# Kernel tuning notes

Hardware: AMD Instinct MI355X
Metric: run time of the kernel (lower is better)

The kernel has to match this reference:

```python
import jax, jax.numpy as jnp
import numpy as np
import math

B, S, E = 8, 1024, 1024
H, D = 8, 1024  # n_heads, d_q=d_k=d_v (must equal S and E per broadcasting in the original)


def setup_inputs() -> dict:
    key = jax.random.key(0)
    ks = jax.random.split(key, 9)
    sc_in = 1.0 / math.sqrt(E)
    inputs = jax.random.normal(ks[0], (B, S, E), dtype=jnp.float32)
    Wq = jax.random.uniform(ks[1], (E, H * D), jnp.float32, -sc_in, sc_in)
    bq = jax.random.uniform(ks[2], (H * D,), jnp.float32, -sc_in, sc_in)
    Wk = jax.random.uniform(ks[3], (E, H * D), jnp.float32, -sc_in, sc_in)
    bk = jax.random.uniform(ks[4], (H * D,), jnp.float32, -sc_in, sc_in)
    Wv = jax.random.uniform(ks[5], (E, H * D), jnp.float32, -sc_in, sc_in)
    bv = jax.random.uniform(ks[6], (H * D,), jnp.float32, -sc_in, sc_in)
    WL = jax.random.uniform(ks[7], (E, H * D), jnp.float32, -sc_in, sc_in)
    bL = jax.random.uniform(ks[8], (H * D,), jnp.float32, -sc_in, sc_in)
    return {"inputs": inputs, "Wq": Wq, "bq": bq, "Wk": Wk, "bk": bk,
            "Wv": Wv, "bv": bv, "WL": WL, "bL": bL}


def reference(inputs, Wq, bq, Wk, bk, Wv, bv, WL, bL):
    b = inputs.shape[0]
    # projections -> [B, H, S, D]
    def proj(W, bias):
        return (inputs @ W + bias).reshape(b, S, H, D).transpose(0, 2, 1, 3)
    q = proj(Wq, bq)
    k = proj(Wk, bk)
    v = proj(Wv, bv)
    # elementwise "kv" score: [B,H,S,D] * [B,H,D,S] (D==S so shapes align) -> [B,H,S,S]
    kv = k * jnp.swapaxes(v, -1, -2) * jnp.float32(1.0 / math.sqrt(D))
    attn = jax.nn.softmax(kv, axis=2)          # softmax over non-standard axis 2
    pooled = jnp.sum(attn * q, axis=2)         # [B, H, S]  (S == E)
    return pooled @ WL + bL                    # [B, H, H*D]
```

## Files before the change

### kernel.cpp

```cpp
#include <hip/hip_runtime.h>
#include <hip/hip_bf16.h>
#include <stdint.h>

typedef __attribute__((ext_vector_type(4))) float  f32x4;
typedef __attribute__((ext_vector_type(4))) float  fvec4;
typedef __attribute__((ext_vector_type(8))) short  bhalf8;
typedef __attribute__((ext_vector_type(4))) short  bhalf4;

typedef const __attribute__((address_space(1))) void glb_void;
typedef __attribute__((address_space(3))) void lds_void;

#define HD 8192
#define KDIM 1024

__device__ __forceinline__ float bf2f(short s) {
  union { float f; uint32_t u; } cv; cv.u = ((uint32_t)(uint16_t)s) << 16; return cv.f;
}
__device__ __forceinline__ short f2bf(float f) {
  union { float f; uint32_t u; } cv; cv.f = f;
  uint32_t u = cv.u;
  uint32_t r = (u + 0x7FFFu + ((u >> 16) & 1u)) >> 16;
  return (short)(uint16_t)r;
}

__global__ void cvt_f32_bf16(const float* __restrict__ in, short* __restrict__ out, int n8) {
  int idx = blockIdx.x * blockDim.x + threadIdx.x;
  if (idx >= n8) return;
  fvec4 a = ((const fvec4*)in)[idx * 2 + 0];
  fvec4 b = ((const fvec4*)in)[idx * 2 + 1];
  bhalf8 o;
  o[0]=f2bf(a[0]); o[1]=f2bf(a[1]); o[2]=f2bf(a[2]); o[3]=f2bf(a[3]);
  o[4]=f2bf(b[0]); o[5]=f2bf(b[1]); o[6]=f2bf(b[2]); o[7]=f2bf(b[3]);
  ((bhalf8*)out)[idx] = o;
}

__global__ __launch_bounds__(256)
void transpose_w(const float* __restrict__ W, short* __restrict__ WT) {
  __shared__ float tile[64][65];
  const int bk = blockIdx.x;
  const int bn = blockIdx.y;
  const int t  = threadIdx.x;
  #pragma unroll
  for (int p = 0; p < 4; ++p) {
    int r = p * 16 + (t >> 4);
    int c = (t & 15) * 4;
    fvec4 v = *(const fvec4*)(W + (size_t)(bk * 64 + r) * HD + bn * 64 + c);
    tile[r][c+0] = v[0]; tile[r][c+1] = v[1]; tile[r][c+2] = v[2]; tile[r][c+3] = v[3];
  }
  __syncthreads();
  #pragma unroll
  for (int p = 0; p < 2; ++p) {
    int rr = p * 32 + (t >> 3);
    int cc = (t & 7) * 8;
    bhalf8 o;
    #pragma unroll
    for (int e = 0; e < 8; ++e) o[e] = f2bf(tile[cc + e][rr]);
    *(bhalf8*)(WT + (size_t)(bn * 64 + rr) * KDIM + bk * 64 + cc) = o;
  }
}

template <bool TRANSPOSED>
__global__ __launch_bounds__(256, 2)
void gemm_proj(const short* __restrict__ A, const short* __restrict__ BT,
               const float* __restrict__ bias, short* __restrict__ C) {
  constexpr int LDC = 136;
  __shared__ alignas(16) short smem[128 * LDC];
  short* As = smem;
  short* Bs = smem + 8192;
  short* Cs = smem;

  const int t    = threadIdx.x;
  const int lane = t & 63;
  const int wave = t >> 6;
  const int bm   = blockIdx.x >> 6;
  const int bn   = blockIdx.x & 63;
  const int wr   = wave >> 1, wc = wave & 1;

  f32x4 acc[4][4];
  #pragma unroll
  for (int i = 0; i < 4; ++i)
    #pragma unroll
    for (int j = 0; j < 4; ++j) acc[i][j] = (f32x4)(0.f);

  const int gslot = ((lane & 7) ^ (lane >> 3)) * 8;
  const short* aRow = A  + (size_t)(bm * 128 + (lane >> 3)) * KDIM + gslot;
  const short* bRow = BT + (size_t)(bn * 128 + (lane >> 3)) * KDIM + gslot;

  const int arow = wr * 64 + (lane & 15);
  const int brow = wc * 64 + (lane & 15);
  const int kbase = (lane >> 4) * 8;
  const int swz  = (lane & 7) * 8;

  for (int kt = 0; kt < 16; ++kt) {
    __syncthreads();
    #pragma unroll
    for (int s = 0; s < 4; ++s) {
      int c = s * 4 + wave;
      __builtin_amdgcn_global_load_lds(
          (glb_void*)(aRow + (size_t)(c * 8) * KDIM + kt * 64),
          (lds_void*)((char*)As + c * 1024), 16, 0, 0);
      __builtin_amdgcn_global_load_lds(
          (glb_void*)(bRow + (size_t)(c * 8) * KDIM + kt * 64),
          (lds_void*)((char*)Bs + c * 1024), 16, 0, 0);
    }
    __syncthreads();
    #pragma unroll
    for (int kk = 0; kk < 2; ++kk) {
      bhalf8 af[4], bfm[4];
      #pragma unroll
      for (int mi = 0; mi < 4; ++mi)
        af[mi] = *(const bhalf8*)(As + (arow + mi * 16) * 64 + ((kk * 32 + kbase) ^ swz));
      #pragma unroll
      for (int ni = 0; ni < 4; ++ni)
        bfm[ni] = *(const bhalf8*)(Bs + (brow + ni * 16) * 64 + ((kk * 32 + kbase) ^ swz));
      #pragma unroll
      for (int mi = 0; mi < 4; ++mi)
        #pragma unroll
        for (int ni = 0; ni < 4; ++ni)
          acc[mi][ni] = __builtin_amdgcn_mfma_f32_16x16x32_bf16(af[mi], bfm[ni], acc[mi][ni], 0, 0, 0);
    }
  }

  __syncthreads();

  float bv4[4];
  #pragma unroll
  for (int ni = 0; ni < 4; ++ni) bv4[ni] = bias[bn * 128 + wc * 64 + ni * 16 + (lane & 15)];

  #pragma unroll
  for (int mi = 0; mi < 4; ++mi) {
    #pragma unroll
    for (int ni = 0; ni < 4; ++ni) {
      const int r0 = wr * 64 + mi * 16 + (lane >> 4) * 4;
      const int cl = wc * 64 + ni * 16 + (lane & 15);
      if (TRANSPOSED) {
        bhalf4 pk;
        #pragma unroll
        for (int e = 0; e < 4; ++e) pk[e] = f2bf(acc[mi][ni][e] + bv4[ni]);
        *(bhalf4*)(Cs + cl * LDC + r0) = pk;
      } else {
        #pragma unroll
        for (int e = 0; e < 4; ++e) Cs[(r0 + e) * LDC + cl] = f2bf(acc[mi][ni][e] + bv4[ni]);
      }
    }
  }
  __syncthreads();

  #pragma unroll
  for (int p = 0; p < 8; ++p) {
    const int row = p * 16 + (t >> 4);
    const int ck  = (t & 15) * 8;
    bhalf8 v = *(const bhalf8*)(Cs + row * LDC + ck);
    if (TRANSPOSED) {
      const int n_g   = bn * 128 + row;
      const int mbase = bm * 128;
      const int bl    = mbase >> 10;
      const int ib    = (mbase & 1023) + ck;
      *(bhalf8*)(C + ((size_t)bl * HD + n_g) * 1024 + ib) = v;
    } else {
      const int m_g = bm * 128 + row;
      *(bhalf8*)(C + (size_t)m_g * HD + bn * 128 + ck) = v;
    }
  }
}

__global__ __launch_bounds__(256)
void pool_softmax(const short* __restrict__ QT, const short* __restrict__ KT,
                  const short* __restrict__ V, float* __restrict__ pooled, int b0) {
  const int t    = threadIdx.x;
  const int lane = t & 63;
  const int wave = t >> 6;
  const int task = blockIdx.x * 4 + wave;
  const int j  = task & 1023;
  const int bh = task >> 10;
  const int bl = bh >> 3, h = bh & 7;
  const size_t n = (size_t)h * 1024 + j;

  const bhalf8* qp = (const bhalf8*)(QT + ((size_t)bl * HD + n) * 1024);
  const bhalf8* kp = (const bhalf8*)(KT + ((size_t)bl * HD + n) * 1024);
  const bhalf8* vp = (const bhalf8*)(V + ((size_t)bl * 1024 + j) * HD + (size_t)h * 1024);

  bhalf8 q0 = qp[lane], q1 = qp[64 + lane];
  bhalf8 k0 = kp[lane], k1 = kp[64 + lane];
  bhalf8 v0 = vp[lane], v1 = vp[64 + lane];

  float q[16], x[16];
  float m = -1e30f;
  #pragma unroll
  for (int e = 0; e < 8; ++e) {
    q[e]     = bf2f(q0[e]);  q[8 + e] = bf2f(q1[e]);
    x[e]     = bf2f(k0[e]) * bf2f(v0[e]) * 0.03125f;
    x[8 + e] = bf2f(k1[e]) * bf2f(v1[e]) * 0.03125f;
  }
  #pragma unroll
  for (int e = 0; e < 16; ++e) m = fmaxf(m, x[e]);
  #pragma unroll
  for (int off = 32; off; off >>= 1) m = fmaxf(m, __shfl_xor(m, off, 64));
  float se = 0.f, sq = 0.f;
  #pragma unroll
  for (int e = 0; e < 16; ++e) { float ex = __expf(x[e] - m); se += ex; sq += ex * q[e]; }
  #pragma unroll
  for (int off = 32; off; off >>= 1) { se += __shfl_xor(se, off, 64); sq += __shfl_xor(sq, off, 64); }
  if (lane == 0) pooled[((size_t)(b0 * 8) + bh) * 1024 + j] = sq / se;
}

__global__ __launch_bounds__(256)
void final_gemm(const float* __restrict__ pooled, const float* __restrict__ WL,
                const float* __restrict__ bL, float* __restrict__ out) {
  __shared__ float sp[1024][8];
  const int t  = threadIdx.x;
  const int bn = blockIdx.x;
  const int mg = blockIdx.y;
  for (int idx = t; idx < 8192; idx += 256) {
    int mm = idx >> 10, k = idx & 1023;
    sp[k][mm] = pooled[(size_t)(mg * 8 + mm) * 1024 + k];
  }
  __syncthreads();
  const int n = bn * 256 + t;
  float acc[8];
  #pragma unroll
  for (int mm = 0; mm < 8; ++mm) acc[mm] = 0.f;
  for (int k = 0; k < 1024; ++k) {
    float w = WL[(size_t)k * HD + n];
    const float* r = &sp[k][0];
    #pragma unroll
    for (int mm = 0; mm < 8; ++mm) acc[mm] = fmaf(r[mm], w, acc[mm]);
  }
  float bb = bL[n];
  #pragma unroll
  for (int mm = 0; mm < 8; ++mm) out[(size_t)(mg * 8 + mm) * HD + n] = acc[mm] + bb;
}

extern "C" void kernel_launch(void* const* d_in, const int* in_sizes, int n_in,
                              void* d_out, int out_size, void* d_ws, size_t ws_size,
                              hipStream_t stream) {
  const float* inputs = (const float*)d_in[0];
  const float* Wq = (const float*)d_in[1];
  const float* bq = (const float*)d_in[2];
  const float* Wk = (const float*)d_in[3];
  const float* bk = (const float*)d_in[4];
  const float* Wv = (const float*)d_in[5];
  const float* bv = (const float*)d_in[6];
  const float* WL = (const float*)d_in[7];
  const float* bL = (const float*)d_in[8];
  float* out = (float*)d_out;

  const size_t MB = 1ull << 20;
  int CB; bool threeW;
  if      (ws_size >= 449 * MB) { CB = 8; threeW = true;  }
  else if (ws_size >= 249 * MB) { CB = 4; threeW = true;  }
  else if (ws_size >= 149 * MB) { CB = 2; threeW = true;  }
  else if (ws_size >=  99 * MB) { CB = 1; threeW = true;  }
  else                          { CB = 1; threeW = false; }

  char* ws = (char*)d_ws;
  short* WT0 = (short*)ws;
  short* WT1 = threeW ? (short*)(ws + 16 * MB) : WT0;
  short* WT2 = threeW ? (short*)(ws + 32 * MB) : WT0;
  char* pp = ws + (threeW ? 48 : 16) * MB;
  short* Abf = (short*)pp;  pp += (size_t)CB * 2  * MB;
  short* QT  = (short*)pp;  pp += (size_t)CB * 16 * MB;
  short* KT  = (short*)pp;  pp += (size_t)CB * 16 * MB;
  short* Vn  = (short*)pp;  pp += (size_t)CB * 16 * MB;
  float* pooled = (float*)pp;

  const float* Wmat[3] = {Wq, Wk, Wv};
  const float* bvec[3] = {bq, bk, bv};
  short*       WTs[3]  = {WT0, WT1, WT2};
  short*       Cout[3] = {QT, KT, Vn};

  dim3 tg(16, 128);
  if (threeW)
    for (int pj = 0; pj < 3; ++pj)
      transpose_w<<<tg, 256, 0, stream>>>(Wmat[pj], WTs[pj]);

  for (int b0 = 0; b0 < 8; b0 += CB) {
    cvt_f32_bf16<<<CB * 512, 256, 0, stream>>>(inputs + ((size_t)b0 << 20), Abf, CB << 17);
    for (int pj = 0; pj < 3; ++pj) {
      if (!threeW)
        transpose_w<<<tg, 256, 0, stream>>>(Wmat[pj], WT0);
      if (pj < 2)
        gemm_proj<true ><<<CB * 512, 256, 0, stream>>>(Abf, WTs[pj], bvec[pj], Cout[pj]);
      else
        gemm_proj<false><<<CB * 512, 256, 0, stream>>>(Abf, WTs[pj], bvec[pj], Cout[pj]);
    }
    pool_softmax<<<CB * 2048, 256, 0, stream>>>(QT, KT, Vn, pooled, b0);
  }
  final_gemm<<<dim3(32, 8), 256, 0, stream>>>(pooled, WL, bL, out);
}
```

Baseline: 576.3 us.

## Add 256x256 pipelined projection GEMM and split-K final GEMM

Adds a 512-thread, 256x256-tile projection GEMM for workspaces large enough to batch two or more items. It double-buffers global_load_lds staging, interleaves it with MFMA quarter-tiles under barriers and raised wave priority, and swizzles the block order. The goal is more data reuse per tile and better overlap of loads with compute than the 128-tile kernel. The final GEMM is also split four ways along K into partial buffers plus a reduce kernel that adds the bias, giving more blocks to fill the GPU. The cost is extra partial-sum traffic and a larger LDS footprint.

```diff
diff --git a/kernel.cpp b/kernel.cpp
--- a/kernel.cpp
+++ b/kernel.cpp
@@ -59,15 +59,180 @@
   }
 }
 
+#define BAR()  __builtin_amdgcn_s_barrier()
+#define SBR()  __builtin_amdgcn_sched_barrier(0)
+#define PRIO1  __builtin_amdgcn_s_setprio(1)
+#define PRIO0  __builtin_amdgcn_s_setprio(0)
+
+#define READ_A(DST, BUF, ROFF)                                                   \
+  _Pragma("unroll") for (int mi = 0; mi < 4; ++mi)                               \
+  _Pragma("unroll") for (int ks = 0; ks < 2; ++ks) {                             \
+    int r_ = arow + (ROFF) + mi * 16;                                            \
+    DST[mi][ks] = *(const bhalf8*)(smem + (BUF)*32768 + r_*64 +                  \
+                                   (((ks*4 + kq) ^ (r_ & 7)) * 8)); }
+#define READ_B(DST, BUF, ROFF)                                                   \
+  _Pragma("unroll") for (int ni = 0; ni < 2; ++ni)                               \
+  _Pragma("unroll") for (int ks = 0; ks < 2; ++ks) {                             \
+    int r_ = brow + (ROFF) + ni * 16;                                            \
+    DST[ni][ks] = *(const bhalf8*)(smem + (BUF)*32768 + 16384 + r_*64 +          \
+                                   (((ks*4 + kq) ^ (r_ & 7)) * 8)); }
+#define STAGE_A(BUF, H, KT)                                                      \
+  _Pragma("unroll") for (int L_ = 0; L_ < 2; ++L_) {                             \
+    __builtin_amdgcn_global_load_lds(                                            \
+      (glb_void*)(Ag + (size_t)((H)*128 + (w*2 + L_)*8) * 1024 + (KT)),          \
+      (lds_void*)((char*)smem + (BUF)*65536 + (H)*16384 + (w*2 + L_)*1024),      \
+      16, 0, 0); }
+#define STAGE_B(BUF, H, KT)                                                      \
+  _Pragma("unroll") for (int L_ = 0; L_ < 2; ++L_) {                             \
+    __builtin_amdgcn_global_load_lds(                                            \
+      (glb_void*)(Bg + (size_t)((H)*128 + (w*2 + L_)*8) * 1024 + (KT)),          \
+      (lds_void*)((char*)smem + (BUF)*65536 + 32768 + (H)*16384 + (w*2+L_)*1024),\
+      16, 0, 0); }
+#define MFMA_Q(MO, NO, AFR, BFR)                                                 \
+  _Pragma("unroll") for (int mi = 0; mi < 4; ++mi)                               \
+  _Pragma("unroll") for (int ni = 0; ni < 2; ++ni)                               \
+  _Pragma("unroll") for (int ks = 0; ks < 2; ++ks)                               \
+    acc[(MO)+mi][(NO)+ni] = __builtin_amdgcn_mfma_f32_16x16x32_bf16(             \
+        AFR[mi][ks], BFR[ni][ks], acc[(MO)+mi][(NO)+ni], 0, 0, 0);
+
+#define KTILE(BUF, DOSB, DOSA, KB, KA, VN) do {                                  \
+  READ_A(a0, BUF, 0); READ_B(b0, BUF, 0);                                        \
+  if (DOSB) { STAGE_B(BUF^1, 0, KB); }                                           \
+  BAR(); SBR(); PRIO1; MFMA_Q(0, 0, a0, b0); PRIO0; SBR(); BAR();                \
+  READ_A(a1, BUF, 64);                                                           \
+  if (DOSB) { STAGE_B(BUF^1, 1, KB); }                                           \
+  BAR(); SBR(); PRIO1; MFMA_Q(4, 0, a1, b0); PRIO0; SBR(); BAR();                \
+  READ_B(b1, BUF, 32);                                                           \
+  if (DOSA) { STAGE_A(BUF, 0, KA); }                                             \
+  BAR(); SBR(); PRIO1; MFMA_Q(0, 2, a0, b1); PRIO0; SBR(); BAR();                \
+  if (DOSA) { STAGE_A(BUF, 1, KA); }                                             \
+  BAR(); SBR(); PRIO1; MFMA_Q(4, 2, a1, b1); PRIO0; SBR();                       \
+  if ((VN) == 4)      asm volatile("s_waitcnt vmcnt(4)" ::: "memory");           \
+  else if ((VN) == 0) asm volatile("s_waitcnt vmcnt(0)" ::: "memory");           \
+  BAR();                                                                         \
+} while (0)
+
+template <bool TRANSPOSED>
+__global__ __launch_bounds__(512, 2)
+void gemm256(const short* __restrict__ A, const short* __restrict__ BT,
+             const float* __restrict__ bias, short* __restrict__ C) {
+  __shared__ alignas(16) short smem[65536];
+  const int t    = threadIdx.x;
+  const int lane = t & 63;
+  const int w    = t >> 6;
+  const int wr   = w >> 2, wc = w & 3;
+  const int kq   = lane >> 4;
+
+  const int nwg = gridDim.x;
+  const int id  = blockIdx.x;
+  const int wg  = (id & 7) * (nwg >> 3) + (id >> 3);
+  const int bm  = wg >> 5;
+  const int bn  = wg & 31;
+
+  const int srow = lane >> 3;
+  const int gk   = ((lane & 7) ^ srow) * 8;
+  const short* Ag = A  + (size_t)(bm * 256 + srow) * 1024 + gk;
+  const short* Bg = BT + (size_t)(bn * 256 + srow) * 1024 + gk;
+
+  const int arow = wr * 128 + (lane & 15);
+  const int brow = wc * 64  + (lane & 15);
+
+  f32x4 acc[8][4];
+  #pragma unroll
+  for (int i = 0; i < 8; ++i)
+    #pragma unroll
+    for (int j = 0; j < 4; ++j) acc[i][j] = (f32x4)(0.f);
+  bhalf8 a0[4][2], a1[4][2], b0[2][2], b1[2][2];
+
+  STAGE_A(0, 0, 0);  STAGE_A(0, 1, 0);
+  STAGE_B(0, 0, 0);  STAGE_B(0, 1, 0);
+  STAGE_A(1, 0, 64); STAGE_A(1, 1, 64);
+  asm volatile("s_waitcnt vmcnt(4)" ::: "memory");
+  BAR();
+
+  #pragma unroll 1
+  for (int t2 = 0; t2 < 8; ++t2) {
+    const bool more = (t2 < 7);
+    KTILE(0, true, more, (2*t2 + 1) * 64, (2*t2 + 2) * 64, more ? 4 : 0);
+    KTILE(1, more, more, (2*t2 + 2) * 64, (2*t2 + 3) * 64, more ? 4 : -1);
+  }
+
+  const int LDM = 264;
+  if (TRANSPOSED) {
+    const int bl   = bm >> 2;
+    const int ioff = (bm & 3) * 256;
+    #pragma unroll 1
+    for (int p = 0; p < 2; ++p) {
+      __syncthreads();
+      if ((wc >> 1) == p) {
+        #pragma unroll
+        for (int ni = 0; ni < 4; ++ni) {
+          float bb = bias[bn * 256 + wc * 64 + ni * 16 + (lane & 15)];
+          int n128 = (wc & 1) * 64 + ni * 16 + (lane & 15);
+          #pragma unroll
+          for (int mi = 0; mi < 8; ++mi) {
+            int mloc = wr * 128 + mi * 16 + kq * 4;
+            bhalf4 pk;
+            #pragma unroll
+            for (int e = 0; e < 4; ++e) pk[e] = f2bf(acc[mi][ni][e] + bb);
+            *(bhalf4*)(smem + n128 * LDM + mloc) = pk;
+          }
+        }
+      }
+      __syncthreads();
+      #pragma unroll
+      for (int r = 0; r < 4; ++r) {
+        int row = r * 32 + (t >> 4);
+        int ck  = (t & 15) * 16;
+        bhalf8 v0 = *(const bhalf8*)(smem + row * LDM + ck);
+        bhalf8 v1 = *(const bhalf8*)(smem + row * LDM + ck + 8);
+        size_t dst = ((size_t)bl * HD + (bn * 256 + p * 128 + row)) * 1024 + ioff + ck;
+        *(bhalf8*)(C + dst) = v0;
+        *(bhalf8*)(C + dst + 8) = v1;
+      }
+    }
+  } else {
+    #pragma unroll 1
+    for (int p = 0; p < 2; ++p) {
+      __syncthreads();
+      if (wr == p) {
+        #pragma unroll
+        for (int ni = 0; ni < 4; ++ni) {
+          float bb = bias[bn * 256 + wc * 64 + ni * 16 + (lane & 15)];
+          int nloc = wc * 64 + ni * 16 + (lane & 15);
+          #pragma unroll
+          for (int mi = 0; mi < 8; ++mi) {
+            int mloc = mi * 16 + kq * 4;
+            #pragma unroll
+            for (int e = 0; e < 4; ++e)
+              smem[(mloc + e) * LDM + nloc] = f2bf(acc[mi][ni][e] + bb);
+          }
+        }
+      }
+      __syncthreads();
+      #pragma unroll
+      for (int r = 0; r < 4; ++r) {
+        int row = r * 32 + (t >> 4);
+        int ck  = (t & 15) * 16;
+        bhalf8 v0 = *(const bhalf8*)(smem + row * LDM + ck);
+        bhalf8 v1 = *(const bhalf8*)(smem + row * LDM + ck + 8);
+        size_t dst = (size_t)(bm * 256 + p * 128 + row) * HD + bn * 256 + ck;
+        *(bhalf8*)(C + dst) = v0;
+        *(bhalf8*)(C + dst + 8) = v1;
+      }
+    }
+  }
+}
+
 template <bool TRANSPOSED>
 __global__ __launch_bounds__(256, 2)
 void gemm_proj(const short* __restrict__ A, const short* __restrict__ BT,
                const float* __restrict__ bias, short* __restrict__ C) {
   constexpr int LDC = 136;
-  __shared__ alignas(16) short smem[128 * LDC];
-  short* As = smem;
-  short* Bs = smem + 8192;
-  short* Cs = smem;
+  __shared__ alignas(16) short smem2[128 * LDC];
+  short* As = smem2;
+  short* Bs = smem2 + 8192;
+  short* Cs = smem2;
 
   const int t    = threadIdx.x;
   const int lane = t & 63;
@@ -205,30 +370,49 @@
 }
 
 __global__ __launch_bounds__(256)
-void final_gemm(const float* __restrict__ pooled, const float* __restrict__ WL,
-                const float* __restrict__ bL, float* __restrict__ out) {
-  __shared__ float sp[1024][8];
+void final_gemm2(const float* __restrict__ pooled, const float* __restrict__ WL,
+                 float* __restrict__ part) {
+  __shared__ float sp[256][8];
   const int t  = threadIdx.x;
   const int bn = blockIdx.x;
   const int mg = blockIdx.y;
-  for (int idx = t; idx < 8192; idx += 256) {
-    int mm = idx >> 10, k = idx & 1023;
-    sp[k][mm] = pooled[(size_t)(mg * 8 + mm) * 1024 + k];
+  const int kc = blockIdx.z;
+  for (int idx = t; idx < 2048; idx += 256) {
+    int mm = idx >> 8, k = idx & 255;
+    sp[k][mm] = pooled[(size_t)(mg * 8 + mm) * 1024 + kc * 256 + k];
   }
   __syncthreads();
   const int n = bn * 256 + t;
   float acc[8];
   #pragma unroll
   for (int mm = 0; mm < 8; ++mm) acc[mm] = 0.f;
-  for (int k = 0; k < 1024; ++k) {
-    float w = WL[(size_t)k * HD + n];
-    const float* r = &sp[k][0];
-    #pragma unroll
-    for (int mm = 0; mm < 8; ++mm) acc[mm] = fmaf(r[mm], w, acc[mm]);
-  }
-  float bb = bL[n];
-  #pragma unroll
-  for (int mm = 0; mm < 8; ++mm) out[(size_t)(mg * 8 + mm) * HD + n] = acc[mm] + bb;
+  const float* wp = WL + (size_t)(kc * 256) * HD + n;
+  #pragma unroll 1
+  for (int k0 = 0; k0 < 256; k0 += 8) {
+    float wv[8];
+    #pragma unroll
+    for (int u = 0; u < 8; ++u) wv[u] = wp[(size_t)(k0 + u) * HD];
+    #pragma unroll
+    for (int u = 0; u < 8; ++u)
+      #pragma unroll
+      for (int mm = 0; mm < 8; ++mm) acc[mm] = fmaf(sp[k0 + u][mm], wv[u], acc[mm]);
+  }
+  #pragma unroll
+  for (int mm = 0; mm < 8; ++mm)
+    part[((size_t)kc * 64 + mg * 8 + mm) * HD + n] = acc[mm];
+}
+
+__global__ __launch_bounds__(256)
+void final_reduce(const float* __restrict__ part, const float* __restrict__ bL,
+                  float* __restrict__ out) {
+  int id = blockIdx.x * 256 + threadIdx.x;
+  const f32x4* p4 = (const f32x4*)part;
+  f32x4 s = p4[id];
+  s = s + p4[131072 + id];
+  s = s + p4[262144 + id];
+  s = s + p4[393216 + id];
+  f32x4 bb = ((const f32x4*)bL)[id & 2047];
+  ((f32x4*)out)[id] = s + bb;
 }
 
 extern "C" void kernel_launch(void* const* d_in, const int* in_sizes, int n_in,
@@ -263,11 +447,13 @@
   short* KT  = (short*)pp;  pp += (size_t)CB * 16 * MB;
   short* Vn  = (short*)pp;  pp += (size_t)CB * 16 * MB;
   float* pooled = (float*)pp;
+  float* part = (float*)QT;
 
   const float* Wmat[3] = {Wq, Wk, Wv};
   const float* bvec[3] = {bq, bk, bv};
   short*       WTs[3]  = {WT0, WT1, WT2};
   short*       Cout[3] = {QT, KT, Vn};
+  const bool   big = (CB >= 2);
 
   dim3 tg(16, 128);
   if (threeW)
@@ -279,12 +465,20 @@
     for (int pj = 0; pj < 3; ++pj) {
       if (!threeW)
         transpose_w<<<tg, 256, 0, stream>>>(Wmat[pj], WT0);
-      if (pj < 2)
-        gemm_proj<true ><<<CB * 512, 256, 0, stream>>>(Abf, WTs[pj], bvec[pj], Cout[pj]);
-      else
-        gemm_proj<false><<<CB * 512, 256, 0, stream>>>(Abf, WTs[pj], bvec[pj], Cout[pj]);
+      if (big) {
+        if (pj < 2)
+          gemm256<true ><<<CB * 128, 512, 0, stream>>>(Abf, WTs[pj], bvec[pj], Cout[pj]);
+        else
+          gemm256<false><<<CB * 128, 512, 0, stream>>>(Abf, WTs[pj], bvec[pj], Cout[pj]);
+      } else {
+        if (pj < 2)
+          gemm_proj<true ><<<CB * 512, 256, 0, stream>>>(Abf, WTs[pj], bvec[pj], Cout[pj]);
+        else
+          gemm_proj<false><<<CB * 512, 256, 0, stream>>>(Abf, WTs[pj], bvec[pj], Cout[pj]);
+      }
     }
     pool_softmax<<<CB * 2048, 256, 0, stream>>>(QT, KT, Vn, pooled, b0);
   }
-  final_gemm<<<dim3(32, 8), 256, 0, stream>>>(pooled, WL, bL, out);
-}
+  final_gemm2<<<dim3(32, 8, 4), 256, 0, stream>>>(pooled, WL, part);
+  final_reduce<<<512, 256, 0, stream>>>(part, bL, out);
+}
```

After: 599.0 us. 1.04x slower.
